# Kernel optimization log

Measured on AMD Instinct MI355X. Metric: run time of the kernel, lower is better.

## Reference

```python
import jax, jax.numpy as jnp
import numpy as np

K = 3
STRIDE = 1
PAD = 1


def setup_inputs() -> dict:
    key = jax.random.key(0)
    k1, k2, k3 = jax.random.split(key, 3)
    N, C, H, W = 4, 256, 64, 64
    outC = 256
    x = jax.random.normal(k1, (N, C, H, W), dtype=jnp.float32)
    # offset/mask conv params (torch inits these to 0; small random makes the test nontrivial)
    conv_offset_w = jax.random.normal(k2, (3 * K * K, C, K, K), dtype=jnp.float32) * 0.01
    conv_offset_b = jnp.zeros((3 * K * K,), dtype=jnp.float32)
    # xavier-normal scale for dcn weight
    fan = C * K * K + outC * K * K
    dcn_weight = jax.random.normal(k3, (outC, C, K, K), dtype=jnp.float32) * np.float32(np.sqrt(2.0 / fan))
    return {"x": x, "conv_offset_w": conv_offset_w, "conv_offset_b": conv_offset_b, "dcn_weight": dcn_weight}


def _dcn(x, w_off, b_off, dcn_weight):
    k, s, p = K, STRIDE, PAD
    N, C, H, W = x.shape
    outC = dcn_weight.shape[0]
    KK = k * k
    # offset/mask prediction conv
    om = jax.lax.conv_general_dilated(
        x, w_off, (s, s), [(p, p), (p, p)],
        dimension_numbers=("NCHW", "OIHW", "NCHW")) + b_off[None, :, None, None]
    offset = om[:, : 2 * KK]
    mask = jax.nn.sigmoid(om[:, 2 * KK:])
    oH = (H + 2 * p - (k - 1)) // s
    oW = (W + 2 * p - (k - 1)) // s
    # pad with an extra row/col at bottom-right so floor+1 indexing is in-bounds (as in torch code)
    px = jnp.pad(x, ((0, 0), (0, 0), (p, p + 1), (p, p + 1)))
    px = jnp.transpose(px, (0, 2, 3, 1))  # (N, H+2p+1, W+2p+1, C)
    offset = jnp.transpose(offset, (0, 2, 3, 1)).reshape(N, oH, oW, KK, 2)  # (...,(y,x))
    mask = jnp.transpose(mask, (0, 2, 3, 1))  # (N, oH, oW, KK)
    base_y = jnp.arange(oH, dtype=jnp.float32) * s + p
    base_x = jnp.arange(oW, dtype=jnp.float32) * s + p
    half = (k - 1) // 2
    inner_y = jnp.repeat(jnp.arange(k, dtype=jnp.float32) - half, k)  # kernel-tap y offsets
    inner_x = jnp.tile(jnp.arange(k, dtype=jnp.float32) - half, k)   # kernel-tap x offsets
    pos_y = base_y[None, :, None, None] + inner_y[None, None, None, :] + offset[..., 0]
    pos_x = base_x[None, None, :, None] + inner_x[None, None, None, :] + offset[..., 1]
    pos_y = jnp.clip(pos_y, 0.0, H + 2 * p - 1.0)
    pos_x = jnp.clip(pos_x, 0.0, W + 2 * p - 1.0)
    y1 = jnp.floor(pos_y)
    x1 = jnp.floor(pos_x)
    y1i = y1.astype(jnp.int32)
    x1i = x1.astype(jnp.int32)
    nidx = jnp.arange(N)[:, None, None, None]
    # bilinear gathers: each (N, oH, oW, KK, C)
    v1 = px[nidx, y1i, x1i]
    v2 = px[nidx, y1i, x1i + 1]
    v3 = px[nidx, y1i + 1, x1i]
    v4 = px[nidx, y1i + 1, x1i + 1]
    lh = (pos_y - y1)[..., None]
    lw = (pos_x - x1)[..., None]
    hh = 1.0 - lh
    hw = 1.0 - lw
    value = hh * hw * v1 + hh * lw * v2 + lh * hw * v3 + lh * lw * v4
    value = value * mask[..., None]  # modulated
    w = dcn_weight.reshape(outC, C, KK)
    # sum over in_C and kernel taps -> NCHW output
    out = jnp.einsum("nhwkc,ock->nohw", value, w)
    return out


def reference(x, conv_offset_w, conv_offset_b, dcn_weight):
    return _dcn(x, conv_offset_w, conv_offset_b, dcn_weight)
```

## Files before the change

### kernel.cpp

```cpp
#include <hip/hip_runtime.h>
#include <type_traits>


typedef __bf16 bf16x8 __attribute__((ext_vector_type(8)));
typedef float  f32x4  __attribute__((ext_vector_type(4)));
typedef unsigned short ushort8 __attribute__((ext_vector_type(8)));
typedef unsigned int   uint4v  __attribute__((ext_vector_type(4)));

#define XBF_OFF   0u
#define WREP_OFF  8388608u
#define WMAIN_OFF 8536064u
#define OM_OFF    9715712u

#define LGKM0_BAR() do { __builtin_amdgcn_s_waitcnt(0xC07F); __builtin_amdgcn_s_barrier(); } while (0)

template <int N> using ic = std::integral_constant<int, N>;

__device__ __forceinline__ unsigned short f2bf(float f) {
  unsigned int u = __float_as_uint(f);
  u += 0x7fffu + ((u >> 16) & 1u);
  return (unsigned short)(u >> 16);
}
__device__ __forceinline__ float bf2f(unsigned short h) {
  return __uint_as_float(((unsigned int)h) << 16);
}

__global__ __launch_bounds__(256) void k_pre(const float* __restrict__ x,
                                             const float* __restrict__ w_off,
                                             const float* __restrict__ dcn_w,
                                             unsigned short* __restrict__ xbf,
                                             unsigned short* __restrict__ wrep,
                                             unsigned short* __restrict__ wmain) {
  __shared__ float tile[32][65];
  __shared__ unsigned short lsh[2304];
  int b = blockIdx.x;
  int t = threadIdx.x;
  if (b < 2048) {
    int n  = b >> 9;
    int cb = (b >> 6) & 7;
    int xb = b & 63;
    int xx  = t & 63;
    int cc0 = t >> 6;
#pragma unroll
    for (int j = 0; j < 8; ++j) {
      int cc = cc0 + j * 4;
      tile[cc][xx] = x[((size_t)(n * 256 + cb * 32 + cc) << 12) + xb * 64 + xx];
    }
    __syncthreads();
    int ccw = t & 31;
    int xw0 = t >> 5;
#pragma unroll
    for (int j = 0; j < 8; ++j) {
      int xw = xw0 + j * 8;
      xbf[((size_t)((n << 12) + xb * 64 + xw)) * 256 + cb * 32 + ccw] = f2bf(tile[ccw][xw]);
    }
  } else {
    int ocb = b - 2048;
    if (ocb < 32) {
      int oc = ocb;
      if (oc >= 27) {
#pragma unroll
        for (int j = 0; j < 9; ++j) wrep[oc * 2304 + j * 256 + t] = 0;
        return;
      }
      const float* base = w_off + (size_t)oc * 2304;
#pragma unroll
      for (int j = 0; j < 9; ++j) lsh[j * 256 + t] = f2bf(base[t * 9 + j]);
      __syncthreads();
#pragma unroll
      for (int j = 0; j < 9; ++j) wrep[oc * 2304 + j * 256 + t] = lsh[j * 256 + t];
    } else {
      int oc = ocb - 32;
      const float* base = dcn_w + (size_t)oc * 2304;
      int oco = ((oc >> 4) << 9) + (oc & 15) * 8;
#pragma unroll
      for (int j = 0; j < 9; ++j) {
        int k = j * 256 + t;
        wmain[((k >> 5) << 13) + oco + (((k >> 3) & 3) << 7) + (k & 7)] =
            f2bf(base[t * 9 + j]);
      }
    }
  }
}

__global__ __launch_bounds__(1024) void k_offconv(const unsigned short* __restrict__ xbf,
                                                  const unsigned short* __restrict__ wrep,
                                                  const float* __restrict__ bias,
                                                  float* __restrict__ om) {
  __shared__ __align__(16) unsigned short SHa[4][2][64 * 64];
  __shared__ __align__(16) unsigned short SHb[4][2][32 * 64];
  int t = threadIdx.x;
  int wave = t >> 6, lane = t & 63;
  int grp = wave >> 2, wv = wave & 3;
  int tg = t & 255;
  int bm = ((blockIdx.x & 7) << 5) + (blockIdx.x >> 3);
  int n = bm >> 6, oy = bm & 63;

  unsigned short (*As)[64 * 64] = SHa[grp];
  unsigned short (*Bs)[32 * 64] = SHb[grp];

  int arow = tg >> 2, acc4 = tg & 3;
  int brow = tg >> 3, bch = tg & 7;

  f32x4 acc0 = {0.f, 0.f, 0.f, 0.f};
  f32x4 acc1 = {0.f, 0.f, 0.f, 0.f};

  ushort8 av[2][2]; ushort8 bv[2];
  auto prefetch = [&](int ktg, auto slotc) {
    constexpr int slot = decltype(slotc)::value;
    int kk = ktg >> 2;
    int c0 = (ktg & 3) * 64;
    int dy = kk / 3 - 1, dx = kk % 3 - 1;
    int yy = oy + dy, xxg = arow + dx;
    bool ok = ((unsigned)yy < 64u) && ((unsigned)xxg < 64u);
    const unsigned short* p = xbf + (size_t)(((n * 64 + yy) * 64 + xxg) * 256 + c0 + acc4 * 16);
#pragma unroll
    for (int g = 0; g < 2; ++g)
      av[slot][g] = ok ? *(const ushort8*)(p + g * 8) : (ushort8){0,0,0,0,0,0,0,0};
    bv[slot] = *(const ushort8*)(wrep + (size_t)brow * 2304 + ktg * 64 + bch * 8);
  };

  int k0 = grp * 9;
  prefetch(k0, ic<0>{});
  prefetch(k0 + 1, ic<1>{});
  int mr = lane & 15, q = lane >> 4;

  auto step = [&](int kt, auto slotc) {
    constexpr int slot = decltype(slotc)::value;
#pragma unroll
    for (int g = 0; g < 2; ++g) {
      int ch = (acc4 * 2 + g) ^ (arow & 7);
      *(ushort8*)&As[slot][arow * 64 + ch * 8] = av[slot][g];
    }
    { int ch = bch ^ (brow & 7);
      *(ushort8*)&Bs[slot][brow * 64 + ch * 8] = bv[slot]; }
    if (kt + 2 < 9) prefetch(k0 + kt + 2, slotc);
    LGKM0_BAR();
#pragma unroll
    for (int kh = 0; kh < 2; ++kh) {
      int coff = ((q + kh * 4) ^ (mr & 7)) * 8;
      bf16x8 a  = *(const bf16x8*)&As[slot][(wv * 16 + mr) * 64 + coff];
      bf16x8 b0 = *(const bf16x8*)&Bs[slot][mr * 64 + coff];
      bf16x8 b1 = *(const bf16x8*)&Bs[slot][(16 + mr) * 64 + coff];
      acc0 = __builtin_amdgcn_mfma_f32_16x16x32_bf16(a, b0, acc0, 0, 0, 0);
      acc1 = __builtin_amdgcn_mfma_f32_16x16x32_bf16(a, b1, acc1, 0, 0, 0);
    }
  };
  for (int kp = 0; kp < 4; ++kp) {
    step(2 * kp, ic<0>{});
    step(2 * kp + 1, ic<1>{});
  }
  step(8, ic<0>{});

  float* scratch = (float*)&SHa[0][0][0];
  __syncthreads();
  if (grp > 0) {
#pragma unroll
    for (int nt = 0; nt < 2; ++nt) {
      f32x4 a = nt ? acc1 : acc0;
#pragma unroll
      for (int rg = 0; rg < 4; ++rg)
        scratch[(grp - 1) * 2048 + (wv * 16 + q * 4 + rg) * 32 + nt * 16 + mr] = a[rg];
    }
  }
  __syncthreads();
  if (grp == 0) {
    int r0 = bm * 64;
#pragma unroll
    for (int nt = 0; nt < 2; ++nt) {
      f32x4 a = nt ? acc1 : acc0;
      int oc = nt * 16 + mr;
      float bvl = (oc < 27) ? bias[oc] : 0.f;
#pragma unroll
      for (int rg = 0; rg < 4; ++rg) {
        int pl = wv * 16 + q * 4 + rg;
        float v = a[rg] + bvl + scratch[pl * 32 + oc] +
                  scratch[2048 + pl * 32 + oc] + scratch[4096 + pl * 32 + oc];
        if (oc >= 18 && oc < 27) v = 1.f / (1.f + __expf(-v));
        om[(r0 + pl) * 32 + oc] = v;
      }
    }
  }
}

__global__ __launch_bounds__(1024, 4) void k_gemm_fused(const unsigned short* __restrict__ xbf,
                                                        const float* __restrict__ om,
                                                        const unsigned short* __restrict__ wB,
                                                        float* __restrict__ out) {
  __shared__ __align__(16) unsigned short Ab[2][64 * 128];
  int t = threadIdx.x;
  int wave = t >> 6, lane = t & 63;
  int bmx = ((blockIdx.x & 7) << 5) + (blockIdx.x >> 3);
  int r0 = bmx * 64;

  if (wave < 8) {
    int mr = lane & 15, q = lane >> 4;
    const unsigned short* Bg = wB + wave * 1024 + lane * 8;
    f32x4 acc[4][2];
#pragma unroll
    for (int mt = 0; mt < 4; ++mt)
#pragma unroll
      for (int nt = 0; nt < 2; ++nt) acc[mt][nt] = (f32x4){0.f, 0.f, 0.f, 0.f};

    bf16x8 bfr[2][4];

    auto issueB = [&](int ks, auto slotc) {
      constexpr int slot = decltype(slotc)::value;
#pragma unroll
      for (int kh = 0; kh < 2; ++kh)
#pragma unroll
        for (int nt = 0; nt < 2; ++nt)
          bfr[slot][kh * 2 + nt] =
              *(const bf16x8*)(Bg + (size_t)(ks * 2 + kh) * 8192 + nt * 512);
    };
    auto mfma64 = [&](auto halfc, auto bufc) {
      constexpr int half = decltype(halfc)::value;
      constexpr int buf  = decltype(bufc)::value;
      __builtin_amdgcn_s_setprio(1);
#pragma unroll
      for (int kh = 0; kh < 2; ++kh) {
        int coff = half * 64 + ((q + kh * 4) ^ (mr & 7)) * 8;
        bf16x8 af[4];
#pragma unroll
        for (int mt = 0; mt < 4; ++mt)
          af[mt] = *(const bf16x8*)&Ab[buf][(mt * 16 + mr) * 128 + coff];
#pragma unroll
        for (int mt = 0; mt < 4; ++mt)
#pragma unroll
          for (int nt = 0; nt < 2; ++nt)
            acc[mt][nt] = __builtin_amdgcn_mfma_f32_16x16x32_bf16(
                af[mt], bfr[half][kh * 2 + nt], acc[mt][nt], 0, 0, 0);
      }
      __builtin_amdgcn_s_setprio(0);
    };

    issueB(0, ic<0>{});
    LGKM0_BAR();
    auto cphase = [&](int p, auto bufc) {
      issueB(2 * p - 1, ic<1>{});
      mfma64(ic<0>{}, bufc);
      if (2 * p < 36) issueB(2 * p, ic<0>{});
      mfma64(ic<1>{}, bufc);
      LGKM0_BAR();
    };
    for (int pp = 0; pp < 9; ++pp) {
      cphase(2 * pp + 1, ic<0>{});
      cphase(2 * pp + 2, ic<1>{});
    }

#pragma unroll
    for (int mt = 0; mt < 4; ++mt)
#pragma unroll
      for (int nt = 0; nt < 2; ++nt) {
        int p = r0 + mt * 16 + q * 4;
        int o = wave * 32 + nt * 16 + mr;
        int nn = p >> 12, pyx = p & 4095;
        *(f32x4*)(out + ((size_t)(nn * 256 + o) << 12) + pyx) = acc[mt][nt];
      }
  } else {
    int pt = t - 512;
    int srow = pt >> 3, sch = (pt & 7) * 8;
    int r = r0 + srow;
    int n = r >> 12, yx = r & 4095, oy = yx >> 6, ox = yx & 63;
    const unsigned short* xb = xbf + (size_t)n * (4096 * 256);
    const float* omr = om + (size_t)r * 32;
    int wchA = (((pt & 7) ^ (srow & 7)) << 3);

    float pv_y, pv_x, pv_m;
    float cw1, cw2, cw3, cw4;
    int a1, a2, a3, a4;
    float wbuf[2][4];
    ushort8 g1[2], g2[2], g3[2], g4[2];

    auto loadom = [&](int kk) {
      pv_y = omr[2 * kk]; pv_x = omr[2 * kk + 1]; pv_m = omr[18 + kk];
    };
    auto params = [&](int kk) {
      float py = (float)(oy + kk / 3) + pv_y;
      float px = (float)(ox + kk % 3) + pv_x;
      float m = pv_m;
      py = fminf(fmaxf(py, 0.f), 65.f);
      px = fminf(fmaxf(px, 0.f), 65.f);
      float fy = floorf(py), fx = floorf(px);
      float ly = py - fy, lx = px - fx;
      float hy = 1.f - ly, hx = 1.f - lx;
      int iy = (int)fy, ix = (int)fx;
      bool yv0 = (iy >= 1) && (iy <= 64);
      bool yv1 = (iy <= 63);
      bool xv0 = (ix >= 1) && (ix <= 64);
      bool xv1 = (ix <= 63);
      int y0 = min(max(iy - 1, 0), 63);
      int y1 = min(iy, 63);
      int x0 = min(max(ix - 1, 0), 63);
      int x1 = min(ix, 63);
      cw1 = (yv0 && xv0) ? hy * hx * m : 0.f;
      cw2 = (yv0 && xv1) ? hy * lx * m : 0.f;
      cw3 = (yv1 && xv0) ? ly * hx * m : 0.f;
      cw4 = (yv1 && xv1) ? ly * lx * m : 0.f;
      a1 = ((y0 << 6) + x0) * 256;
      a2 = ((y0 << 6) + x1) * 256;
      a3 = ((y1 << 6) + x0) * 256;
      a4 = ((y1 << 6) + x1) * 256;
    };

    auto issueA = [&](int ktg, auto slotc) {
      constexpr int slot = decltype(slotc)::value;
      wbuf[slot][0] = cw1; wbuf[slot][1] = cw2; wbuf[slot][2] = cw3; wbuf[slot][3] = cw4;
      int c = (ktg & 3) * 64 + sch;
      g1[slot] = *(const ushort8*)(xb + a1 + c);
      g2[slot] = *(const ushort8*)(xb + a2 + c);
      g3[slot] = *(const ushort8*)(xb + a3 + c);
      g4[slot] = *(const ushort8*)(xb + a4 + c);
    };
    auto blend = [&](auto slotc, auto halfc, auto bufc) {
      constexpr int slot = decltype(slotc)::value;
      constexpr int half = decltype(halfc)::value;
      constexpr int buf  = decltype(bufc)::value;
      uint4v rs;
#pragma unroll
      for (int pp = 0; pp < 4; ++pp) {
        float va = wbuf[slot][0] * bf2f(g1[slot][2 * pp])     + wbuf[slot][1] * bf2f(g2[slot][2 * pp]) +
                   wbuf[slot][2] * bf2f(g3[slot][2 * pp])     + wbuf[slot][3] * bf2f(g4[slot][2 * pp]);
        float vb = wbuf[slot][0] * bf2f(g1[slot][2 * pp + 1]) + wbuf[slot][1] * bf2f(g2[slot][2 * pp + 1]) +
                   wbuf[slot][2] * bf2f(g3[slot][2 * pp + 1]) + wbuf[slot][3] * bf2f(g4[slot][2 * pp + 1]);
        unsigned ua = __float_as_uint(va) + 0x8000u;
        unsigned ub = __float_as_uint(vb) + 0x8000u;
        rs[pp] = __builtin_amdgcn_perm(ub, ua, 0x07060302u);
      }
      *(uint4v*)&Ab[buf][srow * 128 + half * 64 + wchA] = rs;
    };

    loadom(0);
    params(0);
    loadom(1);
    issueA(0, ic<0>{});
    issueA(1, ic<1>{});

    auto pphase = [&](int p, auto bufc) {
      blend(ic<0>{}, ic<0>{}, bufc);
      {
        int ksn = 2 * p + 2;
        if (ksn < 36) {
          if ((ksn & 3) == 0) {
            int kk = ksn >> 2;
            params(kk);
            loadom(kk < 8 ? kk + 1 : 8);
          }
          issueA(ksn, ic<0>{});
        }
      }
      blend(ic<1>{}, ic<1>{}, bufc);
      {
        int ksn = 2 * p + 3;
        if (ksn < 36) issueA(ksn, ic<1>{});
      }
      LGKM0_BAR();
    };
    for (int pp = 0; pp < 9; ++pp) {
      pphase(2 * pp,     ic<0>{});
      pphase(2 * pp + 1, ic<1>{});
    }
    LGKM0_BAR();
  }
}

extern "C" void kernel_launch(void* const* d_in, const int* in_sizes, int n_in,
                              void* d_out, int out_size, void* d_ws, size_t ws_size,
                              hipStream_t stream) {
  const float* x     = (const float*)d_in[0];
  const float* w_off = (const float*)d_in[1];
  const float* b_off = (const float*)d_in[2];
  const float* dcn_w = (const float*)d_in[3];
  float* out = (float*)d_out;
  char* ws = (char*)d_ws;
  unsigned short* xbf   = (unsigned short*)(ws + XBF_OFF);
  unsigned short* wrep  = (unsigned short*)(ws + WREP_OFF);
  unsigned short* wmain = (unsigned short*)(ws + WMAIN_OFF);
  float*          om    = (float*)(ws + OM_OFF);

  k_pre<<<2048 + 288, 256, 0, stream>>>(x, w_off, dcn_w, xbf, wrep, wmain);
  k_offconv<<<256, 1024, 0, stream>>>(xbf, wrep, b_off, om);
  k_gemm_fused<<<256, 1024, 0, stream>>>(xbf, om, wmain, out);
}
```

Before: 114.0 us.

## Fuse offset/mask conv into main deformable GEMM kernel via LDS

Merges the offset/mask prediction convolution into the main fused gather+GEMM kernel. Each block now computes its 64-pixel row of offsets and masks, keeps them in shared memory, and then runs the bilinear gather and GEMM without a global round trip. This removes one kernel launch and the global write and read of the om buffer. In exchange the GEMM kernel uses more LDS (about 104KB), which may lower occupancy, and the offset conv now runs serially before the GEMM inside each block.

```diff
diff --git a/kernel.cpp b/kernel.cpp
--- a/kernel.cpp
+++ b/kernel.cpp
@@ -10,7 +10,6 @@
 #define XBF_OFF   0u
 #define WREP_OFF  8388608u
 #define WMAIN_OFF 8536064u
-#define OM_OFF    9715712u
 
 #define LGKM0_BAR() do { __builtin_amdgcn_s_waitcnt(0xC07F); __builtin_amdgcn_s_barrier(); } while (0)
 
@@ -83,118 +82,115 @@
   }
 }
 
-__global__ __launch_bounds__(1024) void k_offconv(const unsigned short* __restrict__ xbf,
-                                                  const unsigned short* __restrict__ wrep,
-                                                  const float* __restrict__ bias,
-                                                  float* __restrict__ om) {
-  __shared__ __align__(16) unsigned short SHa[4][2][64 * 64];
-  __shared__ __align__(16) unsigned short SHb[4][2][32 * 64];
+__global__ __launch_bounds__(1024, 4) void k_gemm_fused(const unsigned short* __restrict__ xbf,
+                                                        const unsigned short* __restrict__ wrep,
+                                                        const float* __restrict__ bias,
+                                                        const unsigned short* __restrict__ wB,
+                                                        float* __restrict__ out) {
+  __shared__ __align__(16) unsigned char smem[98304];
+  __shared__ __align__(16) float om_lds[64 * 32];
   int t = threadIdx.x;
   int wave = t >> 6, lane = t & 63;
-  int grp = wave >> 2, wv = wave & 3;
-  int tg = t & 255;
   int bm = ((blockIdx.x & 7) << 5) + (blockIdx.x >> 3);
   int n = bm >> 6, oy = bm & 63;
-
-  unsigned short (*As)[64 * 64] = SHa[grp];
-  unsigned short (*Bs)[32 * 64] = SHb[grp];
-
-  int arow = tg >> 2, acc4 = tg & 3;
-  int brow = tg >> 3, bch = tg & 7;
-
-  f32x4 acc0 = {0.f, 0.f, 0.f, 0.f};
-  f32x4 acc1 = {0.f, 0.f, 0.f, 0.f};
-
-  ushort8 av[2][2]; ushort8 bv[2];
-  auto prefetch = [&](int ktg, auto slotc) {
-    constexpr int slot = decltype(slotc)::value;
-    int kk = ktg >> 2;
-    int c0 = (ktg & 3) * 64;
-    int dy = kk / 3 - 1, dx = kk % 3 - 1;
-    int yy = oy + dy, xxg = arow + dx;
-    bool ok = ((unsigned)yy < 64u) && ((unsigned)xxg < 64u);
-    const unsigned short* p = xbf + (size_t)(((n * 64 + yy) * 64 + xxg) * 256 + c0 + acc4 * 16);
-#pragma unroll
-    for (int g = 0; g < 2; ++g)
-      av[slot][g] = ok ? *(const ushort8*)(p + g * 8) : (ushort8){0,0,0,0,0,0,0,0};
-    bv[slot] = *(const ushort8*)(wrep + (size_t)brow * 2304 + ktg * 64 + bch * 8);
-  };
-
-  int k0 = grp * 9;
-  prefetch(k0, ic<0>{});
-  prefetch(k0 + 1, ic<1>{});
   int mr = lane & 15, q = lane >> 4;
 
-  auto step = [&](int kt, auto slotc) {
-    constexpr int slot = decltype(slotc)::value;
-#pragma unroll
-    for (int g = 0; g < 2; ++g) {
-      int ch = (acc4 * 2 + g) ^ (arow & 7);
-      *(ushort8*)&As[slot][arow * 64 + ch * 8] = av[slot][g];
-    }
-    { int ch = bch ^ (brow & 7);
-      *(ushort8*)&Bs[slot][brow * 64 + ch * 8] = bv[slot]; }
-    if (kt + 2 < 9) prefetch(k0 + kt + 2, slotc);
-    LGKM0_BAR();
-#pragma unroll
-    for (int kh = 0; kh < 2; ++kh) {
-      int coff = ((q + kh * 4) ^ (mr & 7)) * 8;
-      bf16x8 a  = *(const bf16x8*)&As[slot][(wv * 16 + mr) * 64 + coff];
-      bf16x8 b0 = *(const bf16x8*)&Bs[slot][mr * 64 + coff];
-      bf16x8 b1 = *(const bf16x8*)&Bs[slot][(16 + mr) * 64 + coff];
-      acc0 = __builtin_amdgcn_mfma_f32_16x16x32_bf16(a, b0, acc0, 0, 0, 0);
-      acc1 = __builtin_amdgcn_mfma_f32_16x16x32_bf16(a, b1, acc1, 0, 0, 0);
-    }
-  };
-  for (int kp = 0; kp < 4; ++kp) {
-    step(2 * kp, ic<0>{});
-    step(2 * kp + 1, ic<1>{});
-  }
-  step(8, ic<0>{});
-
-  float* scratch = (float*)&SHa[0][0][0];
-  __syncthreads();
-  if (grp > 0) {
-#pragma unroll
-    for (int nt = 0; nt < 2; ++nt) {
-      f32x4 a = nt ? acc1 : acc0;
-#pragma unroll
-      for (int rg = 0; rg < 4; ++rg)
-        scratch[(grp - 1) * 2048 + (wv * 16 + q * 4 + rg) * 32 + nt * 16 + mr] = a[rg];
+  {
+    auto SHa = reinterpret_cast<unsigned short (*)[2][64 * 64]>(smem);
+    auto SHb = reinterpret_cast<unsigned short (*)[2][32 * 64]>(smem + 65536);
+    int grp = wave >> 2, wv = wave & 3;
+    int tg = t & 255;
+
+    unsigned short (*As)[64 * 64] = SHa[grp];
+    unsigned short (*Bs)[32 * 64] = SHb[grp];
+
+    int arow = tg >> 2, acc4 = tg & 3;
+    int brow = tg >> 3, bch = tg & 7;
+
+    f32x4 acc0 = {0.f, 0.f, 0.f, 0.f};
+    f32x4 acc1 = {0.f, 0.f, 0.f, 0.f};
+
+    ushort8 av[2][2]; ushort8 bv[2];
+    auto prefetch = [&](int ktg, auto slotc) {
+      constexpr int slot = decltype(slotc)::value;
+      int kk = ktg >> 2;
+      int c0 = (ktg & 3) * 64;
+      int dy = kk / 3 - 1, dx = kk % 3 - 1;
+      int yy = oy + dy, xxg = arow + dx;
+      bool ok = ((unsigned)yy < 64u) && ((unsigned)xxg < 64u);
+      const unsigned short* p = xbf + (size_t)(((n * 64 + yy) * 64 + xxg) * 256 + c0 + acc4 * 16);
+#pragma unroll
+      for (int g = 0; g < 2; ++g)
+        av[slot][g] = ok ? *(const ushort8*)(p + g * 8) : (ushort8){0,0,0,0,0,0,0,0};
+      bv[slot] = *(const ushort8*)(wrep + (size_t)brow * 2304 + ktg * 64 + bch * 8);
+    };
+
+    int k0 = grp * 9;
+    prefetch(k0, ic<0>{});
+    prefetch(k0 + 1, ic<1>{});
+
+    auto step = [&](int kt, auto slotc) {
+      constexpr int slot = decltype(slotc)::value;
+#pragma unroll
+      for (int g = 0; g < 2; ++g) {
+        int ch = (acc4 * 2 + g) ^ (arow & 7);
+        *(ushort8*)&As[slot][arow * 64 + ch * 8] = av[slot][g];
+      }
+      { int ch = bch ^ (brow & 7);
+        *(ushort8*)&Bs[slot][brow * 64 + ch * 8] = bv[slot]; }
+      if (kt + 2 < 9) prefetch(k0 + kt + 2, slotc);
+      LGKM0_BAR();
+#pragma unroll
+      for (int kh = 0; kh < 2; ++kh) {
+        int coff = ((q + kh * 4) ^ (mr & 7)) * 8;
+        bf16x8 a  = *(const bf16x8*)&As[slot][(wv * 16 + mr) * 64 + coff];
+        bf16x8 b0 = *(const bf16x8*)&Bs[slot][mr * 64 + coff];
+        bf16x8 b1 = *(const bf16x8*)&Bs[slot][(16 + mr) * 64 + coff];
+        acc0 = __builtin_amdgcn_mfma_f32_16x16x32_bf16(a, b0, acc0, 0, 0, 0);
+        acc1 = __builtin_amdgcn_mfma_f32_16x16x32_bf16(a, b1, acc1, 0, 0, 0);
+      }
+    };
+    for (int kp = 0; kp < 4; ++kp) {
+      step(2 * kp, ic<0>{});
+      step(2 * kp + 1, ic<1>{});
+    }
+    step(8, ic<0>{});
+
+    float* scratch = (float*)smem;
+    __syncthreads();
+    if (grp > 0) {
+#pragma unroll
+      for (int nt = 0; nt < 2; ++nt) {
+        f32x4 a = nt ? acc1 : acc0;
+#pragma unroll
+        for (int rg = 0; rg < 4; ++rg)
+          scratch[(grp - 1) * 2048 + (wv * 16 + q * 4 + rg) * 32 + nt * 16 + mr] = a[rg];
+      }
+    }
+    __syncthreads();
+    if (grp == 0) {
+#pragma unroll
+      for (int nt = 0; nt < 2; ++nt) {
+        f32x4 a = nt ? acc1 : acc0;
+        int oc = nt * 16 + mr;
+        float bvl = (oc < 27) ? bias[oc] : 0.f;
+#pragma unroll
+        for (int rg = 0; rg < 4; ++rg) {
+          int pl = wv * 16 + q * 4 + rg;
+          float v = a[rg] + bvl + scratch[pl * 32 + oc] +
+                    scratch[2048 + pl * 32 + oc] + scratch[4096 + pl * 32 + oc];
+          if (oc >= 18 && oc < 27) v = 1.f / (1.f + __expf(-v));
+          om_lds[pl * 32 + oc] = v;
+        }
+      }
     }
   }
   __syncthreads();
-  if (grp == 0) {
-    int r0 = bm * 64;
-#pragma unroll
-    for (int nt = 0; nt < 2; ++nt) {
-      f32x4 a = nt ? acc1 : acc0;
-      int oc = nt * 16 + mr;
-      float bvl = (oc < 27) ? bias[oc] : 0.f;
-#pragma unroll
-      for (int rg = 0; rg < 4; ++rg) {
-        int pl = wv * 16 + q * 4 + rg;
-        float v = a[rg] + bvl + scratch[pl * 32 + oc] +
-                  scratch[2048 + pl * 32 + oc] + scratch[4096 + pl * 32 + oc];
-        if (oc >= 18 && oc < 27) v = 1.f / (1.f + __expf(-v));
-        om[(r0 + pl) * 32 + oc] = v;
-      }
-    }
-  }
-}
-
-__global__ __launch_bounds__(1024, 4) void k_gemm_fused(const unsigned short* __restrict__ xbf,
-                                                        const float* __restrict__ om,
-                                                        const unsigned short* __restrict__ wB,
-                                                        float* __restrict__ out) {
-  __shared__ __align__(16) unsigned short Ab[2][64 * 128];
-  int t = threadIdx.x;
-  int wave = t >> 6, lane = t & 63;
-  int bmx = ((blockIdx.x & 7) << 5) + (blockIdx.x >> 3);
-  int r0 = bmx * 64;
+
+  auto Ab = reinterpret_cast<unsigned short (*)[64 * 128]>(smem);
+  int r0 = bm * 64;
 
   if (wave < 8) {
-    int mr = lane & 15, q = lane >> 4;
     const unsigned short* Bg = wB + wave * 1024 + lane * 8;
     f32x4 acc[4][2];
 #pragma unroll
@@ -261,9 +257,9 @@
     int pt = t - 512;
     int srow = pt >> 3, sch = (pt & 7) * 8;
     int r = r0 + srow;
-    int n = r >> 12, yx = r & 4095, oy = yx >> 6, ox = yx & 63;
-    const unsigned short* xb = xbf + (size_t)n * (4096 * 256);
-    const float* omr = om + (size_t)r * 32;
+    int rn = r >> 12, yx = r & 4095, poy = yx >> 6, pox = yx & 63;
+    const unsigned short* xb = xbf + (size_t)rn * (4096 * 256);
+    const float* omr = om_lds + srow * 32;
     int wchA = (((pt & 7) ^ (srow & 7)) << 3);
 
     float pv_y, pv_x, pv_m;
@@ -276,8 +272,8 @@
       pv_y = omr[2 * kk]; pv_x = omr[2 * kk + 1]; pv_m = omr[18 + kk];
     };
     auto params = [&](int kk) {
-      float py = (float)(oy + kk / 3) + pv_y;
-      float px = (float)(ox + kk % 3) + pv_x;
+      float py = (float)(poy + kk / 3) + pv_y;
+      float px = (float)(pox + kk % 3) + pv_x;
       float m = pv_m;
       py = fminf(fmaxf(py, 0.f), 65.f);
       px = fminf(fmaxf(px, 0.f), 65.f);
@@ -376,9 +372,7 @@
   unsigned short* xbf   = (unsigned short*)(ws + XBF_OFF);
   unsigned short* wrep  = (unsigned short*)(ws + WREP_OFF);
   unsigned short* wmain = (unsigned short*)(ws + WMAIN_OFF);
-  float*          om    = (float*)(ws + OM_OFF);
 
   k_pre<<<2048 + 288, 256, 0, stream>>>(x, w_off, dcn_w, xbf, wrep, wmain);
-  k_offconv<<<256, 1024, 0, stream>>>(xbf, wrep, b_off, om);
-  k_gemm_fused<<<256, 1024, 0, stream>>>(xbf, om, wmain, out);
-}
+  k_gemm_fused<<<256, 1024, 0, stream>>>(xbf, wrep, b_off, wmain, out);
+}
```

New measurement: 111.3 us (median of 2 runs). -2.3%, faster.
